# Kernel tuning notes

Hardware: AMD Instinct MI355X
Metric: run time of the kernel (lower is better)

## Reference

```python
import jax, jax.numpy as jnp
import numpy as np

B, T, D, H, G = 256, 1024, 32, 64, 4 * 64  # batch, seq, input, hidden, gates


def setup_inputs() -> dict:
    key = jax.random.key(0)
    ks = jax.random.split(key, 12)
    s = 1.0 / np.sqrt(H)  # PyTorch LSTM default init scale
    return {
        "x": jax.random.normal(ks[0], (B, T, D), dtype=jnp.float32),
        "w_ih_l0": jax.random.normal(ks[1], (G, D), dtype=jnp.float32) * s,
        "w_hh_l0": jax.random.normal(ks[2], (G, H), dtype=jnp.float32) * s,
        "b_ih_l0": jax.random.normal(ks[3], (G,), dtype=jnp.float32) * s,
        "b_hh_l0": jax.random.normal(ks[4], (G,), dtype=jnp.float32) * s,
        "w_ih_l1": jax.random.normal(ks[5], (G, H), dtype=jnp.float32) * s,
        "w_hh_l1": jax.random.normal(ks[6], (G, H), dtype=jnp.float32) * s,
        "b_ih_l1": jax.random.normal(ks[7], (G,), dtype=jnp.float32) * s,
        "b_hh_l1": jax.random.normal(ks[8], (G,), dtype=jnp.float32) * s,
        "w_fc": jax.random.normal(ks[9], (1, H), dtype=jnp.float32) * s,
        "b_fc": jax.random.normal(ks[10], (1,), dtype=jnp.float32) * s,
    }


def _lstm_layer(x, w_ih, w_hh, b_ih, b_hh):
    """x: [B, T, Din] -> h_seq [B, T, H]. PyTorch gate order (i, f, g, o)."""
    # Precompute input contribution for all timesteps in one GEMM.
    gx = jnp.einsum('btd,gd->btg', x, w_ih) + b_ih + b_hh  # [B, T, 4H]
    gx = jnp.swapaxes(gx, 0, 1)  # [T, B, 4H] for scan over time
    h0 = jnp.zeros((x.shape[0], H), dtype=x.dtype)
    c0 = jnp.zeros((x.shape[0], H), dtype=x.dtype)

    def step(carry, g_t):
        h, c = carry
        g = g_t + h @ w_hh.T  # [B, 4H]
        i, f, gg, o = jnp.split(g, 4, axis=-1)
        i = jax.nn.sigmoid(i)
        f = jax.nn.sigmoid(f)
        gg = jnp.tanh(gg)
        o = jax.nn.sigmoid(o)
        c = f * c + i * gg
        h = o * jnp.tanh(c)
        return (h, c), h

    _, h_seq = jax.lax.scan(step, (h0, c0), gx)  # h_seq: [T, B, H]
    return jnp.swapaxes(h_seq, 0, 1)  # [B, T, H]


def reference(x, w_ih_l0, w_hh_l0, b_ih_l0, b_hh_l0,
              w_ih_l1, w_hh_l1, b_ih_l1, b_hh_l1, w_fc, b_fc):
    h1 = _lstm_layer(x, w_ih_l0, w_hh_l0, b_ih_l0, b_hh_l0)
    h2 = _lstm_layer(h1, w_ih_l1, w_hh_l1, b_ih_l1, b_hh_l1)
    last = h2[:, -1, :]  # [B, H]
    logits = last @ w_fc.T + b_fc  # [B, 1]
    return jax.nn.sigmoid(logits)
```

## Files before the change

kernel.cpp:

```cpp
#include <hip/hip_runtime.h>

#define TT 1024
#define DD 32
#define HH 64

typedef __fp16 h2v __attribute__((ext_vector_type(2)));
typedef _Float16 f16x8 __attribute__((ext_vector_type(8)));
typedef float f32x4 __attribute__((ext_vector_type(4)));

struct __attribute__((aligned(16))) H4 { h2v p[4]; };

__device__ __forceinline__ h2v pk(float a, float b) {
    return __builtin_amdgcn_cvt_pkrtz(a, b);
}
__device__ __forceinline__ float fsig(float x) {
    float e = __builtin_amdgcn_exp2f(-1.4426950408889634f * x);
    return __builtin_amdgcn_rcpf(1.0f + e);
}
__device__ __forceinline__ float ftanh(float x) {
    float e = __builtin_amdgcn_exp2f(2.885390081777927f * x);
    return 1.0f - 2.0f * __builtin_amdgcn_rcpf(1.0f + e);
}
__device__ __forceinline__ float pick4(f32x4 c, bool s0, bool s1) {
    float lo = s0 ? c[1] : c[0];
    float hi = s0 ? c[3] : c[2];
    return s1 ? hi : lo;
}
__device__ __forceinline__ f16x8 load_afrag(const float* p) {
    float4 f0 = *(const float4*)p;
    float4 f1 = *(const float4*)(p + 4);
    H4 t;
    t.p[0] = pk(f0.x, f0.y); t.p[1] = pk(f0.z, f0.w);
    t.p[2] = pk(f1.x, f1.y); t.p[3] = pk(f1.z, f1.w);
    return __builtin_bit_cast(f16x8, t);
}
#define MFMA16(A, B, C) __builtin_amdgcn_mfma_f32_16x16x32_f16(A, B, C, 0, 0, 0)

__global__ __launch_bounds__(512) void lstm2_b4(
    const float* __restrict__ x,
    const float* __restrict__ w_ih_l0, const float* __restrict__ w_hh_l0,
    const float* __restrict__ b_ih_l0, const float* __restrict__ b_hh_l0,
    const float* __restrict__ w_ih_l1, const float* __restrict__ w_hh_l1,
    const float* __restrict__ b_ih_l1, const float* __restrict__ b_hh_l1,
    const float* __restrict__ w_fc,   const float* __restrict__ b_fc,
    float* __restrict__ out)
{
    const int bbase = blockIdx.x * 4;
    const int tid  = threadIdx.x;
    const int wave = tid >> 6;
    const int lane = tid & 63;
    const bool isL1 = wave < 4;
    const int js   = wave & 3;
    const int quad = lane >> 4;
    const int bb   = lane & 3;
    const int rsel = (lane >> 2) & 3;
    const int jj   = js*16 + quad*4 + rsel;
    const int mrow = lane & 15;

    __shared__ __attribute__((aligned(16))) __fp16 buf[1280];

    {
        int* bi = (int*)buf;
        bi[tid] = 0;
        if (tid < 128) bi[512 + tid] = 0;
    }

    f16x8 A[16];
    float bs0, bs1, bs2, bs3;
    if (isL1) {
        #pragma unroll
        for (int q = 0; q < 4; ++q) {
            const int g = q*64 + js*16 + mrow;
            A[q*3 + 0] = load_afrag(w_ih_l0 + (size_t)g*DD + quad*8);
            A[q*3 + 1] = load_afrag(w_hh_l0 + (size_t)g*HH + quad*8);
            A[q*3 + 2] = load_afrag(w_hh_l0 + (size_t)g*HH + 32 + quad*8);
        }
        bs0 = b_ih_l0[0*64 + jj] + b_hh_l0[0*64 + jj];
        bs1 = b_ih_l0[1*64 + jj] + b_hh_l0[1*64 + jj];
        bs2 = b_ih_l0[2*64 + jj] + b_hh_l0[2*64 + jj];
        bs3 = b_ih_l0[3*64 + jj] + b_hh_l0[3*64 + jj];
    } else {
        #pragma unroll
        for (int q = 0; q < 4; ++q) {
            const int g = q*64 + js*16 + mrow;
            A[q*4 + 0] = load_afrag(w_ih_l1 + (size_t)g*HH + quad*8);
            A[q*4 + 1] = load_afrag(w_ih_l1 + (size_t)g*HH + 32 + quad*8);
            A[q*4 + 2] = load_afrag(w_hh_l1 + (size_t)g*HH + quad*8);
            A[q*4 + 3] = load_afrag(w_hh_l1 + (size_t)g*HH + 32 + quad*8);
        }
        bs0 = b_ih_l1[0*64 + jj] + b_hh_l1[0*64 + jj];
        bs1 = b_ih_l1[1*64 + jj] + b_hh_l1[1*64 + jj];
        bs2 = b_ih_l1[2*64 + jj] + b_hh_l1[2*64 + jj];
        bs3 = b_ih_l1[3*64 + jj] + b_hh_l1[3*64 + jj];
    }

    const int roff = (bb*4 + quad)*8;
    const int cw   = (isL1 ? 1 : 3) + (jj >> 5);
    const int woff = ((cw*4 + bb)*4 + ((jj & 31) >> 3))*8 + (jj & 7);

    const float* xg = x + (size_t)(bbase + (lane >> 4)) * (TT*DD) + (lane & 15)*2;
    const int sdw = ((lane >> 4)*4 + ((lane & 15) >> 2))*4 + ((lane & 15) & 3);
    float2 xv1 = {0.f, 0.f}, xv2 = {0.f, 0.f};

    __syncthreads();
    if (wave == 7) {
        float2 v0 = *(const float2*)xg;
        ((int*)buf)[sdw] = __builtin_bit_cast(int, pk(v0.x, v0.y));
        xv1 = *(const float2*)(xg + DD);
        xv2 = *(const float2*)(xg + 2*DD);
    }
    __syncthreads();

    const bool s0 = (rsel & 1) != 0;
    const bool s1 = (rsel & 2) != 0;
    float cst = 0.0f;

    for (int t = 0; t <= TT; ++t) {
        const int p = t & 1;
        const __fp16* bc = buf + p*640;
        __fp16* bn = buf + (p ^ 1)*640;
        if (isL1) {
            if (t < TT) {
                f16x8 B0 = *(const f16x8*)(bc + 0*128 + roff);
                f16x8 B1 = *(const f16x8*)(bc + 1*128 + roff);
                f16x8 B2 = *(const f16x8*)(bc + 2*128 + roff);

                f32x4 Z = {0.f, 0.f, 0.f, 0.f};
                f32x4 C0 = Z, C1 = Z, C2 = Z, C3 = Z;
                C0 = MFMA16(A[0], B0, C0); C0 = MFMA16(A[1],  B1, C0); C0 = MFMA16(A[2],  B2, C0);
                C1 = MFMA16(A[3], B0, C1); C1 = MFMA16(A[4],  B1, C1); C1 = MFMA16(A[5],  B2, C1);
                C2 = MFMA16(A[6], B0, C2); C2 = MFMA16(A[7],  B1, C2); C2 = MFMA16(A[8],  B2, C2);
                C3 = MFMA16(A[9], B0, C3); C3 = MFMA16(A[10], B1, C3); C3 = MFMA16(A[11], B2, C3);

                float Si = pick4(C0, s0, s1) + bs0;
                float Sf = pick4(C1, s0, s1) + bs1;
                float Sg = pick4(C2, s0, s1) + bs2;
                float So = pick4(C3, s0, s1) + bs3;

                float ii = fsig(Si), ff = fsig(Sf), oo = fsig(So);
                float gg = ftanh(Sg);
                cst = ff * cst + ii * gg;
                float hv = oo * ftanh(cst);
                bn[woff] = (__fp16)hv;
            }
        } else {
            if (wave == 7 && t < TT) {
                ((int*)bn)[sdw] = __builtin_bit_cast(int, pk(xv1.x, xv1.y));
                xv1 = xv2;
                const int tl = (t + 3 < TT) ? (t + 3) : (TT - 1);
                xv2 = *(const float2*)(xg + (size_t)tl*DD);
            }
            if (t > 0) {
                f16x8 B1 = *(const f16x8*)(bc + 1*128 + roff);
                f16x8 B2 = *(const f16x8*)(bc + 2*128 + roff);
                f16x8 B3 = *(const f16x8*)(bc + 3*128 + roff);
                f16x8 B4 = *(const f16x8*)(bc + 4*128 + roff);

                f32x4 Z = {0.f, 0.f, 0.f, 0.f};
                f32x4 C0 = Z, C1 = Z, C2 = Z, C3 = Z;
                C0 = MFMA16(A[0],  B1, C0); C0 = MFMA16(A[1],  B2, C0);
                C0 = MFMA16(A[2],  B3, C0); C0 = MFMA16(A[3],  B4, C0);
                C1 = MFMA16(A[4],  B1, C1); C1 = MFMA16(A[5],  B2, C1);
                C1 = MFMA16(A[6],  B3, C1); C1 = MFMA16(A[7],  B4, C1);
                C2 = MFMA16(A[8],  B1, C2); C2 = MFMA16(A[9],  B2, C2);
                C2 = MFMA16(A[10], B3, C2); C2 = MFMA16(A[11], B4, C2);
                C3 = MFMA16(A[12], B1, C3); C3 = MFMA16(A[13], B2, C3);
                C3 = MFMA16(A[14], B3, C3); C3 = MFMA16(A[15], B4, C3);

                float Si = pick4(C0, s0, s1) + bs0;
                float Sf = pick4(C1, s0, s1) + bs1;
                float Sg = pick4(C2, s0, s1) + bs2;
                float So = pick4(C3, s0, s1) + bs3;

                float ii = fsig(Si), ff = fsig(Sf), oo = fsig(So);
                float gg = ftanh(Sg);
                cst = ff * cst + ii * gg;
                float hv = oo * ftanh(cst);
                bn[woff] = (__fp16)hv;
            }
        }
        __syncthreads();
    }

    if (wave == 0) {
        const int jg = lane >> 2;
        float s = 0.f;
        #pragma unroll
        for (int u2 = 0; u2 < 4; ++u2) {
            const int j = jg*4 + u2;
            float hval = (float)buf[640 + (((3 + (j >> 5))*4 + bb)*4 + ((j & 31) >> 3))*8 + (j & 7)];
            s += hval * w_fc[j];
        }
        s += __shfl_xor(s, 4);
        s += __shfl_xor(s, 8);
        s += __shfl_xor(s, 16);
        s += __shfl_xor(s, 32);
        if (lane < 4) out[bbase + lane] = fsig(s + b_fc[0]);
    }
}

extern "C" void kernel_launch(void* const* d_in, const int* in_sizes, int n_in,
                              void* d_out, int out_size, void* d_ws, size_t ws_size,
                              hipStream_t stream) {
    lstm2_b4<<<dim3(64), dim3(512), 0, stream>>>(
        (const float*)d_in[0],
        (const float*)d_in[1], (const float*)d_in[2],
        (const float*)d_in[3], (const float*)d_in[4],
        (const float*)d_in[5], (const float*)d_in[6],
        (const float*)d_in[7], (const float*)d_in[8],
        (const float*)d_in[9], (const float*)d_in[10],
        (float*)d_out);
}
```

Measured before the change: 543.8 us.

## Pipeline LSTM layers with 4-slot LDS ring and precomputed input-gate MFMAs

Replaces the double-buffered LDS exchange with a 4-slot ring and software-pipelines each step. The input-dependent MFMAs (x for layer 0, h1 for layer 1) for the next step are issued after the current activations, so only the recurrent MFMAs remain on the critical path between barriers. Biases are folded into the MFMA accumulator init. Layer 1 now runs two steps behind layer 0, and the x loader moves to wave 0. The cost is more LDS, more live accumulator registers, and a longer, more complex loop with extra drain iterations.

```diff
diff --git a/kernel.cpp b/kernel.cpp
--- a/kernel.cpp
+++ b/kernel.cpp
@@ -57,16 +57,17 @@
     const int jj   = js*16 + quad*4 + rsel;
     const int mrow = lane & 15;
 
-    __shared__ __attribute__((aligned(16))) __fp16 buf[1280];
+    __shared__ __attribute__((aligned(16))) __fp16 buf[2560];
 
     {
         int* bi = (int*)buf;
         bi[tid] = 0;
-        if (tid < 128) bi[512 + tid] = 0;
+        bi[512 + tid] = 0;
+        if (tid < 256) bi[1024 + tid] = 0;
     }
 
     f16x8 A[16];
-    float bs0, bs1, bs2, bs3;
+    f32x4 bv0, bv1, bv2, bv3;
     if (isL1) {
         #pragma unroll
         for (int q = 0; q < 4; ++q) {
@@ -75,10 +76,14 @@
             A[q*3 + 1] = load_afrag(w_hh_l0 + (size_t)g*HH + quad*8);
             A[q*3 + 2] = load_afrag(w_hh_l0 + (size_t)g*HH + 32 + quad*8);
         }
-        bs0 = b_ih_l0[0*64 + jj] + b_hh_l0[0*64 + jj];
-        bs1 = b_ih_l0[1*64 + jj] + b_hh_l0[1*64 + jj];
-        bs2 = b_ih_l0[2*64 + jj] + b_hh_l0[2*64 + jj];
-        bs3 = b_ih_l0[3*64 + jj] + b_hh_l0[3*64 + jj];
+        #pragma unroll
+        for (int r = 0; r < 4; ++r) {
+            const int j4 = js*16 + quad*4 + r;
+            bv0[r] = b_ih_l0[0*64 + j4] + b_hh_l0[0*64 + j4];
+            bv1[r] = b_ih_l0[1*64 + j4] + b_hh_l0[1*64 + j4];
+            bv2[r] = b_ih_l0[2*64 + j4] + b_hh_l0[2*64 + j4];
+            bv3[r] = b_ih_l0[3*64 + j4] + b_hh_l0[3*64 + j4];
+        }
     } else {
         #pragma unroll
         for (int q = 0; q < 4; ++q) {
@@ -88,10 +93,14 @@
             A[q*4 + 2] = load_afrag(w_hh_l1 + (size_t)g*HH + quad*8);
             A[q*4 + 3] = load_afrag(w_hh_l1 + (size_t)g*HH + 32 + quad*8);
         }
-        bs0 = b_ih_l1[0*64 + jj] + b_hh_l1[0*64 + jj];
-        bs1 = b_ih_l1[1*64 + jj] + b_hh_l1[1*64 + jj];
-        bs2 = b_ih_l1[2*64 + jj] + b_hh_l1[2*64 + jj];
-        bs3 = b_ih_l1[3*64 + jj] + b_hh_l1[3*64 + jj];
+        #pragma unroll
+        for (int r = 0; r < 4; ++r) {
+            const int j4 = js*16 + quad*4 + r;
+            bv0[r] = b_ih_l1[0*64 + j4] + b_hh_l1[0*64 + j4];
+            bv1[r] = b_ih_l1[1*64 + j4] + b_hh_l1[1*64 + j4];
+            bv2[r] = b_ih_l1[2*64 + j4] + b_hh_l1[2*64 + j4];
+            bv3[r] = b_ih_l1[3*64 + j4] + b_hh_l1[3*64 + j4];
+        }
     }
 
     const int roff = (bb*4 + quad)*8;
@@ -103,84 +112,102 @@
     float2 xv1 = {0.f, 0.f}, xv2 = {0.f, 0.f};
 
     __syncthreads();
-    if (wave == 7) {
+    if (wave == 0) {
         float2 v0 = *(const float2*)xg;
-        ((int*)buf)[sdw] = __builtin_bit_cast(int, pk(v0.x, v0.y));
-        xv1 = *(const float2*)(xg + DD);
-        xv2 = *(const float2*)(xg + 2*DD);
+        ((int*)(buf + 0*640))[sdw] = __builtin_bit_cast(int, pk(v0.x, v0.y));
+        float2 v1 = *(const float2*)(xg + DD);
+        ((int*)(buf + 1*640))[sdw] = __builtin_bit_cast(int, pk(v1.x, v1.y));
+        xv1 = *(const float2*)(xg + 2*DD);
+        xv2 = *(const float2*)(xg + 3*DD);
     }
     __syncthreads();
+
+    f32x4 Ca0 = bv0, Ca1 = bv1, Ca2 = bv2, Ca3 = bv3;
+    f32x4 Cb0 = bv0, Cb1 = bv1, Cb2 = bv2, Cb3 = bv3;
+    if (isL1) {
+        f16x8 B0 = *(const f16x8*)(buf + 0*640 + roff);
+        Ca0 = MFMA16(A[0], B0, bv0);
+        Ca1 = MFMA16(A[3], B0, bv1);
+        Ca2 = MFMA16(A[6], B0, bv2);
+        Ca3 = MFMA16(A[9], B0, bv3);
+    }
 
     const bool s0 = (rsel & 1) != 0;
     const bool s1 = (rsel & 2) != 0;
     float cst = 0.0f;
 
-    for (int t = 0; t <= TT; ++t) {
-        const int p = t & 1;
-        const __fp16* bc = buf + p*640;
-        __fp16* bn = buf + (p ^ 1)*640;
-        if (isL1) {
-            if (t < TT) {
-                f16x8 B0 = *(const f16x8*)(bc + 0*128 + roff);
-                f16x8 B1 = *(const f16x8*)(bc + 1*128 + roff);
-                f16x8 B2 = *(const f16x8*)(bc + 2*128 + roff);
-
-                f32x4 Z = {0.f, 0.f, 0.f, 0.f};
-                f32x4 C0 = Z, C1 = Z, C2 = Z, C3 = Z;
-                C0 = MFMA16(A[0], B0, C0); C0 = MFMA16(A[1],  B1, C0); C0 = MFMA16(A[2],  B2, C0);
-                C1 = MFMA16(A[3], B0, C1); C1 = MFMA16(A[4],  B1, C1); C1 = MFMA16(A[5],  B2, C1);
-                C2 = MFMA16(A[6], B0, C2); C2 = MFMA16(A[7],  B1, C2); C2 = MFMA16(A[8],  B2, C2);
-                C3 = MFMA16(A[9], B0, C3); C3 = MFMA16(A[10], B1, C3); C3 = MFMA16(A[11], B2, C3);
-
-                float Si = pick4(C0, s0, s1) + bs0;
-                float Sf = pick4(C1, s0, s1) + bs1;
-                float Sg = pick4(C2, s0, s1) + bs2;
-                float So = pick4(C3, s0, s1) + bs3;
-
-                float ii = fsig(Si), ff = fsig(Sf), oo = fsig(So);
-                float gg = ftanh(Sg);
-                cst = ff * cst + ii * gg;
-                float hv = oo * ftanh(cst);
-                bn[woff] = (__fp16)hv;
-            }
-        } else {
-            if (wave == 7 && t < TT) {
-                ((int*)bn)[sdw] = __builtin_bit_cast(int, pk(xv1.x, xv1.y));
-                xv1 = xv2;
-                const int tl = (t + 3 < TT) ? (t + 3) : (TT - 1);
-                xv2 = *(const float2*)(xg + (size_t)tl*DD);
-            }
-            if (t > 0) {
-                f16x8 B1 = *(const f16x8*)(bc + 1*128 + roff);
-                f16x8 B2 = *(const f16x8*)(bc + 2*128 + roff);
-                f16x8 B3 = *(const f16x8*)(bc + 3*128 + roff);
-                f16x8 B4 = *(const f16x8*)(bc + 4*128 + roff);
-
-                f32x4 Z = {0.f, 0.f, 0.f, 0.f};
-                f32x4 C0 = Z, C1 = Z, C2 = Z, C3 = Z;
-                C0 = MFMA16(A[0],  B1, C0); C0 = MFMA16(A[1],  B2, C0);
-                C0 = MFMA16(A[2],  B3, C0); C0 = MFMA16(A[3],  B4, C0);
-                C1 = MFMA16(A[4],  B1, C1); C1 = MFMA16(A[5],  B2, C1);
-                C1 = MFMA16(A[6],  B3, C1); C1 = MFMA16(A[7],  B4, C1);
-                C2 = MFMA16(A[8],  B1, C2); C2 = MFMA16(A[9],  B2, C2);
-                C2 = MFMA16(A[10], B3, C2); C2 = MFMA16(A[11], B4, C2);
-                C3 = MFMA16(A[12], B1, C3); C3 = MFMA16(A[13], B2, C3);
-                C3 = MFMA16(A[14], B3, C3); C3 = MFMA16(A[15], B4, C3);
-
-                float Si = pick4(C0, s0, s1) + bs0;
-                float Sf = pick4(C1, s0, s1) + bs1;
-                float Sg = pick4(C2, s0, s1) + bs2;
-                float So = pick4(C3, s0, s1) + bs3;
-
-                float ii = fsig(Si), ff = fsig(Sf), oo = fsig(So);
-                float gg = ftanh(Sg);
-                cst = ff * cst + ii * gg;
-                float hv = oo * ftanh(cst);
-                bn[woff] = (__fp16)hv;
-            }
-        }
-        __syncthreads();
-    }
+#define ACT_WRITE(SLOT, C0_, C1_, C2_, C3_)                                   \
+    {   float Si = pick4(C0_, s0, s1);                 \
+        float Sf = pick4(C1_, s0, s1);                                        \
+        float Sg = pick4(C2_, s0, s1);                                        \
+        float So = pick4(C3_, s0, s1);                                        \
+        float ii = fsig(Si), ff = fsig(Sf), oo = fsig(So);                    \
+        float gg = ftanh(Sg);                                                 \
+        cst = ff * cst + ii * gg;                                             \
+        float hv = oo * ftanh(cst);                                           \
+        buf[(SLOT)*640 + woff] = (__fp16)hv;                                  \
+    }
+
+#define STEP(K, P0,P1,P2,P3, Q0,Q1,Q2,Q3)                                     \
+    {   const int t = tb + (K);                                               \
+        if (wave == 0 && (t + 2 < TT)) {      \
+            ((int*)(buf + (((K)+2)&3)*640))[sdw] =                            \
+                __builtin_bit_cast(int, pk(xv1.x, xv1.y));                    \
+            xv1 = xv2;                                                        \
+            const int tl = (t + 4 < TT) ? (t + 4) : (TT - 1);                 \
+            xv2 = *(const float2*)(xg + (size_t)tl*DD);                       \
+        }                                                                     \
+        if (isL1) {                                                           \
+            if (t < TT) {                     \
+                const __fp16* bp = buf + (((K)-1)&3)*640;                     \
+                f16x8 B1 = *(const f16x8*)(bp + 128 + roff);                  \
+                f16x8 B2 = *(const f16x8*)(bp + 256 + roff);                  \
+                P0 = MFMA16(A[1],  B1, P0); P0 = MFMA16(A[2],  B2, P0);       \
+                P1 = MFMA16(A[4],  B1, P1); P1 = MFMA16(A[5],  B2, P1);       \
+                P2 = MFMA16(A[7],  B1, P2); P2 = MFMA16(A[8],  B2, P2);       \
+                P3 = MFMA16(A[10], B1, P3); P3 = MFMA16(A[11], B2, P3);       \
+                ACT_WRITE((K)&3, P0, P1, P2, P3);                             \
+            }                                                                 \
+            if (t < TT - 1) {                    \
+                f16x8 B0 = *(const f16x8*)(buf + (((K)+1)&3)*640 + roff);     \
+                Q0 = MFMA16(A[0], B0, bv0);                                   \
+                Q1 = MFMA16(A[3], B0, bv1);                                   \
+                Q2 = MFMA16(A[6], B0, bv2);                                   \
+                Q3 = MFMA16(A[9], B0, bv3);                                   \
+            }                                                                 \
+        } else {                                                              \
+            if (t >= 2 && t <= TT + 1) {      \
+                const __fp16* bp = buf + (((K)-3)&3)*640;                     \
+                f16x8 B3 = *(const f16x8*)(bp + 384 + roff);                  \
+                f16x8 B4 = *(const f16x8*)(bp + 512 + roff);                  \
+                P0 = MFMA16(A[2],  B3, P0); P0 = MFMA16(A[3],  B4, P0);       \
+                P1 = MFMA16(A[6],  B3, P1); P1 = MFMA16(A[7],  B4, P1);       \
+                P2 = MFMA16(A[10], B3, P2); P2 = MFMA16(A[11], B4, P2);       \
+                P3 = MFMA16(A[14], B3, P3); P3 = MFMA16(A[15], B4, P3);       \
+                ACT_WRITE(((K)-2)&3, P0, P1, P2, P3);            \
+            }                                                                 \
+            if (t >= 1 && t <= TT) {            \
+                const __fp16* bp = buf + (((K)-1)&3)*640;                     \
+                f16x8 B1 = *(const f16x8*)(bp + 128 + roff);                  \
+                f16x8 B2 = *(const f16x8*)(bp + 256 + roff);                  \
+                Q0 = MFMA16(A[0],  B1, bv0); Q0 = MFMA16(A[1],  B2, Q0);      \
+                Q1 = MFMA16(A[4],  B1, bv1); Q1 = MFMA16(A[5],  B2, Q1);      \
+                Q2 = MFMA16(A[8],  B1, bv2); Q2 = MFMA16(A[9],  B2, Q2);      \
+                Q3 = MFMA16(A[12], B1, bv3); Q3 = MFMA16(A[13], B2, Q3);      \
+            }                                                                 \
+        }                                                                     \
+        __syncthreads();                                                      \
+    }
+
+    for (int tb = 0; tb < TT + 4; tb += 4) {
+        STEP(0, Ca0,Ca1,Ca2,Ca3, Cb0,Cb1,Cb2,Cb3)
+        STEP(1, Cb0,Cb1,Cb2,Cb3, Ca0,Ca1,Ca2,Ca3)
+        STEP(2, Ca0,Ca1,Ca2,Ca3, Cb0,Cb1,Cb2,Cb3)
+        STEP(3, Cb0,Cb1,Cb2,Cb3, Ca0,Ca1,Ca2,Ca3)
+    }
+
+#undef STEP
+#undef ACT_WRITE
 
     if (wave == 0) {
         const int jg = lane >> 2;
@@ -188,7 +215,8 @@
         #pragma unroll
         for (int u2 = 0; u2 < 4; ++u2) {
             const int j = jg*4 + u2;
-            float hval = (float)buf[640 + (((3 + (j >> 5))*4 + bb)*4 + ((j & 31) >> 3))*8 + (j & 7)];
+            float hval = (float)buf[3*640 +
+                (((3 + (j >> 5))*4 + bb)*4 + ((j & 31) >> 3))*8 + (j & 7)];
             s += hval * w_fc[j];
         }
         s += __shfl_xor(s, 4);
```

New measurement: 561.9 us. 1.03x slower.

## Remap LSTM to one batch element per block with one wave per layer

Applied to the files above, without the earlier changes.

Replaces the 64-block design, where each block handled four batch elements across eight waves, with 256 blocks of two waves each. Each block handles one batch element: one wave runs layer 0 and the other runs layer 1, lagging by one step. Each wave keeps all gate weight tiles in registers and issues 48–64 MFMAs per step instead of 12–16. The aim is to use all CUs and to synchronise only two waves per step, at the cost of a longer per-wave MFMA chain and very high register use. The x loads are also prefetched two steps ahead directly into the layer-0 wave, and the loop is unrolled by two to alternate the h1 buffers.

```diff
diff --git a/kernel.cpp b/kernel.cpp
--- a/kernel.cpp
+++ b/kernel.cpp
@@ -36,7 +36,27 @@
 }
 #define MFMA16(A, B, C) __builtin_amdgcn_mfma_f32_16x16x32_f16(A, B, C, 0, 0, 0)
 
-__global__ __launch_bounds__(512) void lstm2_b4(
+__device__ __forceinline__ void mrow(f32x4 (&C)[16], const f16x8 (&A)[16], f16x8 Bv) {
+#pragma unroll
+    for (int mt = 0; mt < 16; ++mt) C[mt] = MFMA16(A[mt], Bv, C[mt]);
+}
+__device__ __forceinline__ void mrowz(f32x4 (&C)[16], const f16x8 (&A)[16], f16x8 Bv, f32x4 zv) {
+#pragma unroll
+    for (int mt = 0; mt < 16; ++mt) C[mt] = MFMA16(A[mt], Bv, zv);
+}
+template<int G>
+__device__ __forceinline__ float selg(const f32x4 (&C)[16],
+                                      bool s0, bool s1, bool s2, bool s3) {
+    float ta = pick4(C[0*4 + G],  s0, s1);
+    float tb = pick4(C[1*4 + G],  s0, s1);
+    float tc = pick4(C[2*4 + G],  s0, s1);
+    float td = pick4(C[3*4 + G],  s0, s1);
+    float tl = s2 ? tb : ta;
+    float th = s2 ? td : tc;
+    return s3 ? th : tl;
+}
+
+__global__ __launch_bounds__(128, 1) void lstm2_pair(
     const float* __restrict__ x,
     const float* __restrict__ w_ih_l0, const float* __restrict__ w_hh_l0,
     const float* __restrict__ b_ih_l0, const float* __restrict__ b_hh_l0,
@@ -45,164 +65,148 @@
     const float* __restrict__ w_fc,   const float* __restrict__ b_fc,
     float* __restrict__ out)
 {
-    const int bbase = blockIdx.x * 4;
+    const int b    = blockIdx.x;
     const int tid  = threadIdx.x;
     const int wave = tid >> 6;
     const int lane = tid & 63;
-    const bool isL1 = wave < 4;
-    const int js   = wave & 3;
     const int quad = lane >> 4;
-    const int bb   = lane & 3;
-    const int rsel = (lane >> 2) & 3;
-    const int jj   = js*16 + quad*4 + rsel;
-    const int mrow = lane & 15;
-
-    __shared__ __attribute__((aligned(16))) __fp16 buf[1280];
-
-    {
-        int* bi = (int*)buf;
-        bi[tid] = 0;
-        if (tid < 128) bi[512 + tid] = 0;
-    }
-
-    f16x8 A[16];
+    const int mr   = lane & 15;
+    const bool s0 = (lane & 1) != 0;
+    const bool s1 = (lane & 2) != 0;
+    const bool s2 = (lane & 4) != 0;
+    const bool s3 = (lane & 8) != 0;
+    const int jlane = ((lane >> 2) & 3)*16 + quad*4 + (lane & 3);
+
+    __shared__ __attribute__((aligned(16))) __fp16 h1buf[2][64];
+    __shared__ __attribute__((aligned(16))) __fp16 h2buf[64];
+
+    if (tid < 64) {
+        h1buf[0][tid] = (__fp16)0.f;
+        h1buf[1][tid] = (__fp16)0.f;
+        h2buf[tid]    = (__fp16)0.f;
+    }
+
+    f16x8 W0[16], W1[16], W2[16], W3[16];
     float bs0, bs1, bs2, bs3;
-    if (isL1) {
+    if (wave == 0) {
         #pragma unroll
-        for (int q = 0; q < 4; ++q) {
-            const int g = q*64 + js*16 + mrow;
-            A[q*3 + 0] = load_afrag(w_ih_l0 + (size_t)g*DD + quad*8);
-            A[q*3 + 1] = load_afrag(w_hh_l0 + (size_t)g*HH + quad*8);
-            A[q*3 + 2] = load_afrag(w_hh_l0 + (size_t)g*HH + 32 + quad*8);
+        for (int mt = 0; mt < 16; ++mt) {
+            const int G = (mt & 3)*64 + (mt >> 2)*16 + mr;
+            W0[mt] = load_afrag(w_ih_l0 + (size_t)G*DD + quad*8);
+            W1[mt] = load_afrag(w_hh_l0 + (size_t)G*HH + quad*8);
+            W2[mt] = load_afrag(w_hh_l0 + (size_t)G*HH + 32 + quad*8);
+            W3[mt] = W0[mt];
         }
-        bs0 = b_ih_l0[0*64 + jj] + b_hh_l0[0*64 + jj];
-        bs1 = b_ih_l0[1*64 + jj] + b_hh_l0[1*64 + jj];
-        bs2 = b_ih_l0[2*64 + jj] + b_hh_l0[2*64 + jj];
-        bs3 = b_ih_l0[3*64 + jj] + b_hh_l0[3*64 + jj];
+        bs0 = b_ih_l0[0*64 + jlane] + b_hh_l0[0*64 + jlane];
+        bs1 = b_ih_l0[1*64 + jlane] + b_hh_l0[1*64 + jlane];
+        bs2 = b_ih_l0[2*64 + jlane] + b_hh_l0[2*64 + jlane];
+        bs3 = b_ih_l0[3*64 + jlane] + b_hh_l0[3*64 + jlane];
     } else {
         #pragma unroll
-        for (int q = 0; q < 4; ++q) {
-            const int g = q*64 + js*16 + mrow;
-            A[q*4 + 0] = load_afrag(w_ih_l1 + (size_t)g*HH + quad*8);
-            A[q*4 + 1] = load_afrag(w_ih_l1 + (size_t)g*HH + 32 + quad*8);
-            A[q*4 + 2] = load_afrag(w_hh_l1 + (size_t)g*HH + quad*8);
-            A[q*4 + 3] = load_afrag(w_hh_l1 + (size_t)g*HH + 32 + quad*8);
+        for (int mt = 0; mt < 16; ++mt) {
+            const int G = (mt & 3)*64 + (mt >> 2)*16 + mr;
+            W0[mt] = load_afrag(w_ih_l1 + (size_t)G*HH + quad*8);
+            W1[mt] = load_afrag(w_ih_l1 + (size_t)G*HH + 32 + quad*8);
+            W2[mt] = load_afrag(w_hh_l1 + (size_t)G*HH + quad*8);
+            W3[mt] = load_afrag(w_hh_l1 + (size_t)G*HH + 32 + quad*8);
         }
-        bs0 = b_ih_l1[0*64 + jj] + b_hh_l1[0*64 + jj];
-        bs1 = b_ih_l1[1*64 + jj] + b_hh_l1[1*64 + jj];
-        bs2 = b_ih_l1[2*64 + jj] + b_hh_l1[2*64 + jj];
-        bs3 = b_ih_l1[3*64 + jj] + b_hh_l1[3*64 + jj];
-    }
-
-    const int roff = (bb*4 + quad)*8;
-    const int cw   = (isL1 ? 1 : 3) + (jj >> 5);
-    const int woff = ((cw*4 + bb)*4 + ((jj & 31) >> 3))*8 + (jj & 7);
-
-    const float* xg = x + (size_t)(bbase + (lane >> 4)) * (TT*DD) + (lane & 15)*2;
-    const int sdw = ((lane >> 4)*4 + ((lane & 15) >> 2))*4 + ((lane & 15) & 3);
-    float2 xv1 = {0.f, 0.f}, xv2 = {0.f, 0.f};
+        bs0 = b_ih_l1[0*64 + jlane] + b_hh_l1[0*64 + jlane];
+        bs1 = b_ih_l1[1*64 + jlane] + b_hh_l1[1*64 + jlane];
+        bs2 = b_ih_l1[2*64 + jlane] + b_hh_l1[2*64 + jlane];
+        bs3 = b_ih_l1[3*64 + jlane] + b_hh_l1[3*64 + jlane];
+    }
+
+    const float* xrow = x + (size_t)b*(TT*DD) + quad*8;
+    float4 xa0 = {0,0,0,0}, xa1 = {0,0,0,0}, xb0 = {0,0,0,0}, xb1 = {0,0,0,0};
+    if (wave == 0) {
+        xa0 = *(const float4*)(xrow + 0*DD);
+        xa1 = *(const float4*)(xrow + 0*DD + 4);
+        xb0 = *(const float4*)(xrow + 1*DD);
+        xb1 = *(const float4*)(xrow + 1*DD + 4);
+    }
 
     __syncthreads();
-    if (wave == 7) {
-        float2 v0 = *(const float2*)xg;
-        ((int*)buf)[sdw] = __builtin_bit_cast(int, pk(v0.x, v0.y));
-        xv1 = *(const float2*)(xg + DD);
-        xv2 = *(const float2*)(xg + 2*DD);
-    }
-    __syncthreads();
-
-    const bool s0 = (rsel & 1) != 0;
-    const bool s1 = (rsel & 2) != 0;
+
+    const f32x4 zv = {0.f, 0.f, 0.f, 0.f};
     float cst = 0.0f;
 
-    for (int t = 0; t <= TT; ++t) {
-        const int p = t & 1;
-        const __fp16* bc = buf + p*640;
-        __fp16* bn = buf + (p ^ 1)*640;
-        if (isL1) {
-            if (t < TT) {
-                f16x8 B0 = *(const f16x8*)(bc + 0*128 + roff);
-                f16x8 B1 = *(const f16x8*)(bc + 1*128 + roff);
-                f16x8 B2 = *(const f16x8*)(bc + 2*128 + roff);
-
-                f32x4 Z = {0.f, 0.f, 0.f, 0.f};
-                f32x4 C0 = Z, C1 = Z, C2 = Z, C3 = Z;
-                C0 = MFMA16(A[0], B0, C0); C0 = MFMA16(A[1],  B1, C0); C0 = MFMA16(A[2],  B2, C0);
-                C1 = MFMA16(A[3], B0, C1); C1 = MFMA16(A[4],  B1, C1); C1 = MFMA16(A[5],  B2, C1);
-                C2 = MFMA16(A[6], B0, C2); C2 = MFMA16(A[7],  B1, C2); C2 = MFMA16(A[8],  B2, C2);
-                C3 = MFMA16(A[9], B0, C3); C3 = MFMA16(A[10], B1, C3); C3 = MFMA16(A[11], B2, C3);
-
-                float Si = pick4(C0, s0, s1) + bs0;
-                float Sf = pick4(C1, s0, s1) + bs1;
-                float Sg = pick4(C2, s0, s1) + bs2;
-                float So = pick4(C3, s0, s1) + bs3;
-
-                float ii = fsig(Si), ff = fsig(Sf), oo = fsig(So);
-                float gg = ftanh(Sg);
-                cst = ff * cst + ii * gg;
-                float hv = oo * ftanh(cst);
-                bn[woff] = (__fp16)hv;
-            }
-        } else {
-            if (wave == 7 && t < TT) {
-                ((int*)bn)[sdw] = __builtin_bit_cast(int, pk(xv1.x, xv1.y));
-                xv1 = xv2;
-                const int tl = (t + 3 < TT) ? (t + 3) : (TT - 1);
-                xv2 = *(const float2*)(xg + (size_t)tl*DD);
-            }
-            if (t > 0) {
-                f16x8 B1 = *(const f16x8*)(bc + 1*128 + roff);
-                f16x8 B2 = *(const f16x8*)(bc + 2*128 + roff);
-                f16x8 B3 = *(const f16x8*)(bc + 3*128 + roff);
-                f16x8 B4 = *(const f16x8*)(bc + 4*128 + roff);
-
-                f32x4 Z = {0.f, 0.f, 0.f, 0.f};
-                f32x4 C0 = Z, C1 = Z, C2 = Z, C3 = Z;
-                C0 = MFMA16(A[0],  B1, C0); C0 = MFMA16(A[1],  B2, C0);
-                C0 = MFMA16(A[2],  B3, C0); C0 = MFMA16(A[3],  B4, C0);
-                C1 = MFMA16(A[4],  B1, C1); C1 = MFMA16(A[5],  B2, C1);
-                C1 = MFMA16(A[6],  B3, C1); C1 = MFMA16(A[7],  B4, C1);
-                C2 = MFMA16(A[8],  B1, C2); C2 = MFMA16(A[9],  B2, C2);
-                C2 = MFMA16(A[10], B3, C2); C2 = MFMA16(A[11], B4, C2);
-                C3 = MFMA16(A[12], B1, C3); C3 = MFMA16(A[13], B2, C3);
-                C3 = MFMA16(A[14], B3, C3); C3 = MFMA16(A[15], B4, C3);
-
-                float Si = pick4(C0, s0, s1) + bs0;
-                float Sf = pick4(C1, s0, s1) + bs1;
-                float Sg = pick4(C2, s0, s1) + bs2;
-                float So = pick4(C3, s0, s1) + bs3;
-
-                float ii = fsig(Si), ff = fsig(Sf), oo = fsig(So);
-                float gg = ftanh(Sg);
-                cst = ff * cst + ii * gg;
-                float hv = oo * ftanh(cst);
-                bn[woff] = (__fp16)hv;
-            }
-        }
-        __syncthreads();
-    }
-
-    if (wave == 0) {
+#define ACT_H(C)                                                              \
+        float Si = selg<0>(C, s0, s1, s2, s3) + bs0;                          \
+        float Sf = selg<1>(C, s0, s1, s2, s3) + bs1;                          \
+        float Sg = selg<2>(C, s0, s1, s2, s3) + bs2;                          \
+        float So = selg<3>(C, s0, s1, s2, s3) + bs3;                          \
+        float ii = fsig(Si), ff = fsig(Sf), oo = fsig(So);                    \
+        float gg = ftanh(Sg);                                                 \
+        cst = ff * cst + ii * gg;                                             \
+        float hv = oo * ftanh(cst);
+
+#define STEP(I_, PAR, X0_, X1_)                                               \
+    {   const int i = (I_);                                                   \
+        if (wave == 0) {                                                      \
+            if (i < TT) {                                                     \
+                f16x8 Bx; { H4 u;                                             \
+                    u.p[0] = pk(X0_.x, X0_.y); u.p[1] = pk(X0_.z, X0_.w);     \
+                    u.p[2] = pk(X1_.x, X1_.y); u.p[3] = pk(X1_.z, X1_.w);     \
+                    Bx = __builtin_bit_cast(f16x8, u); }                      \
+                {   const int tl = (i + 2 < TT) ? (i + 2) : (TT - 1);         \
+                    X0_ = *(const float4*)(xrow + (size_t)tl*DD);             \
+                    X1_ = *(const float4*)(xrow + (size_t)tl*DD + 4); }       \
+                f32x4 C[16];                                                  \
+                mrowz(C, W0, Bx, zv);                                         \
+                f16x8 D1 = *(const f16x8*)(&h1buf[(PAR)^1][0] + quad*8);      \
+                f16x8 D2 = *(const f16x8*)(&h1buf[(PAR)^1][0] + 32 + quad*8); \
+                mrow(C, W1, D1);                                              \
+                mrow(C, W2, D2);                                              \
+                ACT_H(C)                                                      \
+                h1buf[PAR][jlane] = (__fp16)hv;                               \
+            }                                                                 \
+        } else {                                                              \
+            if (i >= 1) {                                                     \
+                f16x8 B1 = *(const f16x8*)(&h1buf[(PAR)^1][0] + quad*8);      \
+                f16x8 B2 = *(const f16x8*)(&h1buf[(PAR)^1][0] + 32 + quad*8); \
+                f16x8 D1 = *(const f16x8*)(h2buf + quad*8);                   \
+                f16x8 D2 = *(const f16x8*)(h2buf + 32 + quad*8);              \
+                f32x4 C[16];                                                  \
+                mrowz(C, W0, B1, zv);                                         \
+                mrow(C, W1, B2);                                              \
+                mrow(C, W2, D1);                                              \
+                mrow(C, W3, D2);                                              \
+                ACT_H(C)                                                      \
+                h2buf[jlane] = (__fp16)hv;                                    \
+            }                                                                 \
+        }                                                                     \
+        __syncthreads();                                                      \
+    }
+
+    for (int tb = 0; tb < TT; tb += 2) {
+        STEP(tb,     0, xa0, xa1)
+        STEP(tb + 1, 1, xb0, xb1)
+    }
+    STEP(TT, 0, xa0, xa1)
+
+#undef STEP
+#undef ACT_H
+
+    if (wave == 1) {
         const int jg = lane >> 2;
         float s = 0.f;
         #pragma unroll
         for (int u2 = 0; u2 < 4; ++u2) {
             const int j = jg*4 + u2;
-            float hval = (float)buf[640 + (((3 + (j >> 5))*4 + bb)*4 + ((j & 31) >> 3))*8 + (j & 7)];
-            s += hval * w_fc[j];
+            s += (float)h2buf[j] * w_fc[j];
         }
         s += __shfl_xor(s, 4);
         s += __shfl_xor(s, 8);
         s += __shfl_xor(s, 16);
         s += __shfl_xor(s, 32);
-        if (lane < 4) out[bbase + lane] = fsig(s + b_fc[0]);
+        if (lane == 0) out[b] = fsig(s + b_fc[0]);
     }
 }
 
 extern "C" void kernel_launch(void* const* d_in, const int* in_sizes, int n_in,
                               void* d_out, int out_size, void* d_ws, size_t ws_size,
                               hipStream_t stream) {
-    lstm2_b4<<<dim3(64), dim3(512), 0, stream>>>(
+    lstm2_pair<<<dim3(256), dim3(128), 0, stream>>>(
         (const float*)d_in[0],
         (const float*)d_in[1], (const float*)d_in[2],
         (const float*)d_in[3], (const float*)d_in[4],
```

Result: slower. 1.027 ms (+88.8%).
